# Performance work log

Hardware: AMD Instinct MI355X
Metric: run time of the kernel (lower is better)

The kernel has to match this reference:

```python
import jax, jax.numpy as jnp
import numpy as np

HIDDEN = 4544
NUM_HEADS = 71
HEAD_DIM = 64
ROPE_BASE = 10000.0


def _rope_cos_sin(seq_len, dim, dtype):
    inv_freq = 1.0 / (ROPE_BASE ** (jnp.arange(0, dim, 2, dtype=jnp.float32) / dim))
    t = jnp.arange(seq_len, dtype=jnp.float32)
    freqs = jnp.einsum('i,j->ij', t, inv_freq)            # [S, dim/2]
    emb = jnp.concatenate([freqs, freqs], axis=-1)        # [S, dim]
    return jnp.cos(emb).astype(dtype), jnp.sin(emb).astype(dtype)


def _rotate_half(x):
    half = x.shape[-1] // 2
    return jnp.concatenate([-x[..., half:], x[..., :half]], axis=-1)


def _apply_rope(x, cos, sin):
    # x: [..., S, hd]; cos/sin: [S, hd]
    return x * cos + _rotate_half(x) * sin


def setup_inputs() -> dict:
    key = jax.random.key(0)
    k1, k2, k3 = jax.random.split(key, 3)
    B, S = 1, 1024
    hidden_states = jax.random.normal(k1, (B, 1, S, HIDDEN), dtype=jnp.float32) * 0.02
    # additive causal mask (prefill)
    neg = jnp.triu(jnp.full((S, S), -1e9, dtype=jnp.float32), k=1)
    attention_mask = jnp.broadcast_to(neg[None, None], (B, 1, S, S))
    # fused QKV weight (already transposed for right-matmul): [H, (nh+2)*hd]
    qkv_w = jax.random.normal(k2, (HIDDEN, (NUM_HEADS + 2) * HEAD_DIM), dtype=jnp.float32) * 0.02
    dense_w = jax.random.normal(k3, (HIDDEN, HIDDEN), dtype=jnp.float32) * 0.02
    return {"hidden_states": hidden_states, "attention_mask": attention_mask,
            "qkv_w": qkv_w, "dense_w": dense_w}


def reference(hidden_states, attention_mask, qkv_w, dense_w):
    B, _, S, H = hidden_states.shape
    nh, hd = NUM_HEADS, HEAD_DIM
    x = hidden_states[:, 0]                               # [B, S, H]
    fused = jnp.einsum('bsh,hf->bsf', x, qkv_w)           # [B, S, (nh+2)*hd]
    fused = fused.reshape(B, S, nh + 2, hd)
    q = jnp.transpose(fused[:, :, :nh, :], (0, 2, 1, 3))  # [B, nh, S, hd]
    k = fused[:, :, nh, :]                                # [B, S, hd]  (single KV head, MQA)
    v = fused[:, :, nh + 1, :]                            # [B, S, hd]
    cos, sin = _rope_cos_sin(S, hd, q.dtype)
    q = _apply_rope(q, cos, sin)
    k = _apply_rope(k, cos, sin)
    scale = 1.0 / np.sqrt(hd).astype(np.float32)
    scores = jnp.einsum('bhsd,btd->bhst', q, k) * scale   # [B, nh, S, S]
    scores = scores + attention_mask                      # broadcast over heads
    probs = jax.nn.softmax(scores, axis=-1)
    ctx = jnp.einsum('bhst,btd->bhsd', probs, v)          # [B, nh, S, hd]
    ctx = jnp.transpose(ctx, (0, 2, 1, 3)).reshape(B, S, nh * hd)
    out = jnp.einsum('bsh,hg->bsg', ctx, dense_w)         # [B, S, H]
    return out[:, None]                                   # [B, 1, S, H]
```

## Files before the change

kernel.cpp:

```cpp
#include <hip/hip_runtime.h>

#define S_LEN 1024
#define HID   4544
#define NH    71
#define NQKV  4672

typedef __attribute__((ext_vector_type(4))) float f32x4;
typedef __attribute__((ext_vector_type(4))) unsigned short u16x4;
typedef __attribute__((ext_vector_type(8))) unsigned short u16x8;
typedef __attribute__((ext_vector_type(8))) __bf16 bf16x8;

__device__ __forceinline__ bf16x8 as_bf(u16x8 v) { return __builtin_bit_cast(bf16x8, v); }

__device__ __forceinline__ unsigned short f2bf(float f) {
    unsigned u = __builtin_bit_cast(unsigned, f);
    return (unsigned short)((u + 0x7FFFu + ((u >> 16) & 1u)) >> 16);
}
__device__ __forceinline__ float bf2f(unsigned short u) {
    return __builtin_bit_cast(float, (unsigned)u << 16);
}
__device__ __forceinline__ unsigned pk2(float a, float b) {
    return (unsigned)f2bf(a) | ((unsigned)f2bf(b) << 16);
}
__device__ __forceinline__ void gload16(const void* g, void* l) {
    __builtin_amdgcn_global_load_lds((const __attribute__((address_space(1))) unsigned int*)g,
                                     (__attribute__((address_space(3))) unsigned int*)l,
                                     16, 0, 0);
}

__global__ __launch_bounds__(256) void cvt_x_kernel(const float4* __restrict__ x,
                                                    ushort4* __restrict__ y) {
    int i = blockIdx.x * 256 + threadIdx.x;
    float4 v = x[i];
    ushort4 r;
    r.x = f2bf(v.x); r.y = f2bf(v.y); r.z = f2bf(v.z); r.w = f2bf(v.w);
    y[i] = r;
}

__global__ __launch_bounds__(256) void cvt_wT_kernel(const float* __restrict__ w,
                                                     unsigned short* __restrict__ wt,
                                                     int K, int N) {
    __shared__ float t[64][65];
    int n0 = blockIdx.x * 64, k0 = blockIdx.y * 64;
    int tx = threadIdx.x & 15, ty = threadIdx.x >> 4;
#pragma unroll
    for (int r = 0; r < 64; r += 16) {
        int k = k0 + ty + r;
        float4 v = *(const float4*)&w[(size_t)k * N + n0 + tx * 4];
        t[ty + r][tx * 4 + 0] = v.x;
        t[ty + r][tx * 4 + 1] = v.y;
        t[ty + r][tx * 4 + 2] = v.z;
        t[ty + r][tx * 4 + 3] = v.w;
    }
    __syncthreads();
    int nr = threadIdx.x >> 2;
    int kq = (threadIdx.x & 3) * 16;
    unsigned short tmp[16];
#pragma unroll
    for (int z = 0; z < 16; z++) tmp[z] = f2bf(t[kq + z][nr]);
    u16x8* dst = (u16x8*)&wt[(size_t)(n0 + nr) * K + k0 + kq];
    dst[0] = *(const u16x8*)&tmp[0];
    dst[1] = *(const u16x8*)&tmp[8];
}

__global__ void rope_table_kernel(float* __restrict__ cs, float* __restrict__ sn) {
    int s = blockIdx.x, i = threadIdx.x;
    float inv = powf(10000.0f, -(2.0f * (float)i) / 64.0f);
    float f = (float)s * inv;
    cs[s * 32 + i] = cosf(f);
    sn[s * 32 + i] = sinf(f);
}

template<int EPI>
__global__ __launch_bounds__(256, 3) void gemm_bt_kernel(
        const unsigned short* __restrict__ A, const unsigned short* __restrict__ BT,
        void* __restrict__ Cout, const float* __restrict__ cs_t,
        const float* __restrict__ sn_t, unsigned short* __restrict__ k_out,
        unsigned short* __restrict__ v_out, int K, int ldc) {
    __shared__ unsigned short As[2][128 * 64];
    __shared__ unsigned short Bs[2][64 * 64];
    int m0 = blockIdx.y * 128, n0 = blockIdx.x * 64;
    int t = threadIdx.x;
    int wv = t >> 6, lane = t & 63, lr = lane & 15, lg = lane >> 4;
    int mw = wv * 32;
    int sw = lr & 7;
    int srow = t >> 3, sc16 = t & 7;

    f32x4 acc[2][4];
#pragma unroll
    for (int mi = 0; mi < 2; mi++)
#pragma unroll
        for (int ni = 0; ni < 4; ni++) acc[mi][ni] = (f32x4)0.0f;

    const char* Ab = (const char*)A;
    const char* Bb = (const char*)BT;
    size_t rs = (size_t)K * 2;

    auto stage = [&](int step, int buf) {
        size_t kb = (size_t)step * 128;
#pragma unroll
        for (int i = 0; i < 4; i++) {
            int row = i * 32 + srow;
            int csrc = sc16 ^ (row & 7);
            gload16(Ab + (size_t)(m0 + row) * rs + kb + csrc * 16,
                    (char*)As[buf] + (i * 256 + t) * 16);
        }
#pragma unroll
        for (int i = 0; i < 2; i++) {
            int row = i * 32 + srow;
            int csrc = sc16 ^ (row & 7);
            gload16(Bb + (size_t)(n0 + row) * rs + kb + csrc * 16,
                    (char*)Bs[buf] + (i * 256 + t) * 16);
        }
    };

    stage(0, 0);
    __syncthreads();
    int nsteps = K >> 6;
    for (int s = 0; s < nsteps; ++s) {
        int cur = s & 1;
        if (s + 1 < nsteps) stage(s + 1, cur ^ 1);
        bf16x8 af[2][2], bfr[4][2];
#pragma unroll
        for (int mi = 0; mi < 2; mi++)
#pragma unroll
            for (int kk = 0; kk < 2; kk++) {
                int row = mw + mi * 16 + lr;
                af[mi][kk] = as_bf(*(const u16x8*)&As[cur][row * 64 + (((kk * 4 + lg) ^ sw) << 3)]);
            }
#pragma unroll
        for (int ni = 0; ni < 4; ni++)
#pragma unroll
            for (int kk = 0; kk < 2; kk++) {
                int row = ni * 16 + lr;
                bfr[ni][kk] = as_bf(*(const u16x8*)&Bs[cur][row * 64 + (((kk * 4 + lg) ^ sw) << 3)]);
            }
#pragma unroll
        for (int mi = 0; mi < 2; mi++)
#pragma unroll
            for (int ni = 0; ni < 4; ni++) {
                acc[mi][ni] = __builtin_amdgcn_mfma_f32_16x16x32_bf16(af[mi][0], bfr[ni][0], acc[mi][ni], 0, 0, 0);
                acc[mi][ni] = __builtin_amdgcn_mfma_f32_16x16x32_bf16(af[mi][1], bfr[ni][1], acc[mi][ni], 0, 0, 0);
            }
        __syncthreads();
    }

    if (EPI == 0) {
        float* C = (float*)Cout;
#pragma unroll
        for (int mi = 0; mi < 2; mi++)
#pragma unroll
            for (int ni = 0; ni < 4; ni++) {
                int col = n0 + ni * 16 + lr;
#pragma unroll
                for (int i = 0; i < 4; i++) {
                    int row = m0 + mw + mi * 16 + 4 * lg + i;
                    C[(size_t)row * ldc + col] = acc[mi][ni][i];
                }
            }
    } else {
        int hh = blockIdx.x;
        if (hh == 72) {
#pragma unroll
            for (int mi = 0; mi < 2; mi++)
#pragma unroll
                for (int ni = 0; ni < 4; ni++) {
                    int d = ni * 16 + lr;
                    int s0 = m0 + mw + mi * 16 + 4 * lg;
                    u16x4 pk;
#pragma unroll
                    for (int i = 0; i < 4; i++) pk[i] = f2bf(acc[mi][ni][i]);
                    *(u16x4*)&v_out[(size_t)d * S_LEN + s0] = pk;
                }
        } else {
            unsigned short* qb = (unsigned short*)Cout;
            float qscale = (hh < 71) ? 0.125f : 1.0f;
#pragma unroll
            for (int mi = 0; mi < 2; mi++)
#pragma unroll
                for (int i = 0; i < 4; i++) {
                    int s = m0 + mw + mi * 16 + 4 * lg + i;
                    float c0 = cs_t[s * 32 + lr],      g0 = sn_t[s * 32 + lr];
                    float c1 = cs_t[s * 32 + 16 + lr], g1 = sn_t[s * 32 + 16 + lr];
#pragma unroll
                    for (int ni = 0; ni < 4; ni++) {
                        float x  = acc[mi][ni][i];
                        float xp = acc[mi][ni ^ 2][i];
                        float c = (ni & 1) ? c1 : c0;
                        float g = (ni & 1) ? g1 : g0;
                        float r = (ni < 2) ? (x * c - xp * g) : (x * c + xp * g);
                        r *= qscale;
                        int d = ni * 16 + lr;
                        if (hh < 71) qb[(size_t)s * HID + hh * 64 + d] = f2bf(r);
                        else         k_out[(size_t)s * 64 + d] = f2bf(r);
                    }
                }
        }
    }
}

__global__ __launch_bounds__(256, 3) void attn_kernel(
        const unsigned short* __restrict__ qb, const unsigned short* __restrict__ kr,
        const unsigned short* __restrict__ vt, unsigned short* __restrict__ ctx,
        unsigned short* __restrict__ Opart, float2* __restrict__ MLpart) {
    __shared__ unsigned short Ks[2][64 * 64];
    __shared__ unsigned short Vs[2][64 * 64];
    __shared__ unsigned short Pl[4][16 * 72];
    int h = blockIdx.y;
    int u = blockIdx.x;
    int c, j0;
    if (u < 16)      { c = 0; j0 = u * 4; }
    else if (u < 28) { c = 1; j0 = 16 + (u - 16) * 4; }
    else if (u < 36) { c = 2; j0 = 32 + (u - 28) * 4; }
    else             { c = 3; j0 = 48 + (u - 36) * 4; }
    int t = threadIdx.x, wv = t >> 6, lane = t & 63, lr = lane & 15, lg = lane >> 4;
    int j = j0 + wv;
    int qs = j * 16 + lr;
    int k_lo = c * 256;
    int kend_w   = min((j + 1) * 16, k_lo + 256);
    int kend_max = min((j0 + 4) * 16, k_lo + 256);
    int nt = (kend_max - k_lo) >> 6;
    int nch = (j >> 4) + 1;
    int srow = t >> 3, sc16 = t & 7, sw = lr & 7;

    auto stage = [&](int ti, int buf) {
        size_t kbase = (size_t)(k_lo + ti * 64);
#pragma unroll
        for (int i = 0; i < 2; i++) {
            int row = i * 32 + srow;
            int csrc = sc16 ^ (row & 7);
            gload16((const char*)kr + (kbase + row) * 128 + csrc * 16,
                    (char*)Ks[buf] + (i * 256 + t) * 16);
        }
#pragma unroll
        for (int i = 0; i < 2; i++) {
            int row = i * 32 + srow;
            int csrc = sc16 ^ (row & 7);
            gload16((const char*)vt + (size_t)row * 2048 + kbase * 2 + csrc * 16,
                    (char*)Vs[buf] + (i * 256 + t) * 16);
        }
    };

    bf16x8 qf[2];
#pragma unroll
    for (int dc = 0; dc < 2; dc++)
        qf[dc] = as_bf(*(const u16x8*)&qb[(size_t)qs * HID + h * 64 + dc * 32 + 8 * lg]);

    float m_i = -1e30f, l_i = 0.0f;
    f32x4 o[4];
#pragma unroll
    for (int d4 = 0; d4 < 4; d4++) o[d4] = (f32x4)0.0f;

    stage(0, 0);
    __syncthreads();

    for (int ti = 0; ti < nt; ti++) {
        int cur = ti & 1;
        if (ti + 1 < nt) stage(ti + 1, cur ^ 1);
        int k0 = k_lo + ti * 64;
        if (k0 < kend_w) {
            f32x4 st[4];
#pragma unroll
            for (int nc = 0; nc < 4; nc++) st[nc] = (f32x4)0.0f;
#pragma unroll
            for (int nc = 0; nc < 4; nc++) {
                int krow = nc * 16 + lr;
#pragma unroll
                for (int dc = 0; dc < 2; dc++) {
                    bf16x8 kf = as_bf(*(const u16x8*)&Ks[cur][krow * 64 + (((dc * 4 + lg) ^ sw) << 3)]);
                    st[nc] = __builtin_amdgcn_mfma_f32_16x16x32_bf16(kf, qf[dc], st[nc], 0, 0, 0);
                }
            }
            bool needmask = (k0 + 64 > j * 16);
            float mx = -1e30f;
            if (needmask) {
#pragma unroll
                for (int nc = 0; nc < 4; nc++)
#pragma unroll
                    for (int i = 0; i < 4; i++) {
                        int ks = k0 + nc * 16 + 4 * lg + i;
                        float v = (ks <= qs) ? st[nc][i] : -1e30f;
                        st[nc][i] = v;
                        mx = fmaxf(mx, v);
                    }
            } else {
#pragma unroll
                for (int nc = 0; nc < 4; nc++)
#pragma unroll
                    for (int i = 0; i < 4; i++) mx = fmaxf(mx, st[nc][i]);
            }
            mx = fmaxf(mx, __shfl_xor(mx, 16));
            mx = fmaxf(mx, __shfl_xor(mx, 32));
            if (!__all(mx <= m_i + 8.0f)) {
                float mn = fmaxf(m_i, mx);
                float so = __expf(m_i - mn);
                l_i *= so;
#pragma unroll
                for (int d4 = 0; d4 < 4; d4++)
#pragma unroll
                    for (int i = 0; i < 4; i++) o[d4][i] *= so;
                m_i = mn;
            }
            float ps = 0.0f;
#pragma unroll
            for (int nc = 0; nc < 4; nc++)
#pragma unroll
                for (int i = 0; i < 4; i++) {
                    float v = st[nc][i];
                    float e = (!needmask || v > -1e29f) ? __expf(v - m_i) : 0.0f;
                    st[nc][i] = e;
                    ps += e;
                }
            ps += __shfl_xor(ps, 16);
            ps += __shfl_xor(ps, 32);
            l_i += ps;
#pragma unroll
            for (int nc = 0; nc < 4; nc++) {
                *(unsigned*)&Pl[wv][lr * 72 + nc * 16 + 4 * lg]     = pk2(st[nc][0], st[nc][1]);
                *(unsigned*)&Pl[wv][lr * 72 + nc * 16 + 4 * lg + 2] = pk2(st[nc][2], st[nc][3]);
            }
            bf16x8 pb[2];
#pragma unroll
            for (int kk = 0; kk < 2; kk++)
                pb[kk] = as_bf(*(const u16x8*)&Pl[wv][lr * 72 + kk * 32 + 8 * lg]);
#pragma unroll
            for (int d4 = 0; d4 < 4; d4++) {
                int vrow = d4 * 16 + lr;
#pragma unroll
                for (int kk = 0; kk < 2; kk++) {
                    bf16x8 vf = as_bf(*(const u16x8*)&Vs[cur][vrow * 64 + (((kk * 4 + lg) ^ sw) << 3)]);
                    o[d4] = __builtin_amdgcn_mfma_f32_16x16x32_bf16(vf, pb[kk], o[d4], 0, 0, 0);
                }
            }
        }
        __syncthreads();
    }

    if (nch == 1) {
        float linv = 1.0f / l_i;
#pragma unroll
        for (int d4 = 0; d4 < 4; d4++) {
            u16x4 pk;
#pragma unroll
            for (int i = 0; i < 4; i++) pk[i] = f2bf(o[d4][i] * linv);
            *(u16x4*)&ctx[(size_t)qs * HID + h * 64 + d4 * 16 + 4 * lg] = pk;
        }
    } else {
        int pi = (h * 48 + (j - 16)) * 4 + c;
#pragma unroll
        for (int d4 = 0; d4 < 4; d4++) {
            u16x4 pk;
#pragma unroll
            for (int i = 0; i < 4; i++) pk[i] = f2bf(o[d4][i]);
            *(u16x4*)&Opart[(size_t)pi * 1024 + lr * 64 + d4 * 16 + 4 * lg] = pk;
        }
        if (lg == 0) MLpart[pi * 16 + lr] = make_float2(m_i, l_i);
    }
}

__global__ __launch_bounds__(256) void merge_kernel(
        const unsigned short* __restrict__ Opart, const float2* __restrict__ MLpart,
        unsigned short* __restrict__ ctx) {
    int mu = blockIdx.x * 4 + (threadIdx.x >> 6);
    int lane = threadIdx.x & 63;
    int h = mu / 48, jj = mu % 48, j = 16 + jj;
    int nch = (j >> 4) + 1;
    int base = (h * 48 + jj) * 4;
    for (int q = 0; q < 16; q++) {
        float m[4], l[4], w[4];
        float M = -1e30f;
        for (int c = 0; c < nch; c++) {
            float2 ml = MLpart[(base + c) * 16 + q];
            m[c] = ml.x; l[c] = ml.y;
            M = fmaxf(M, m[c]);
        }
        float L = 0.0f;
        for (int c = 0; c < nch; c++) { w[c] = __expf(m[c] - M); L += l[c] * w[c]; }
        float acc = 0.0f;
        for (int c = 0; c < nch; c++)
            acc += w[c] * bf2f(Opart[(size_t)(base + c) * 1024 + q * 64 + lane]);
        ctx[(size_t)(j * 16 + q) * HID + h * 64 + lane] = f2bf(acc / L);
    }
}

extern "C" void kernel_launch(void* const* d_in, const int* in_sizes, int n_in,
                              void* d_out, int out_size, void* d_ws, size_t ws_size,
                              hipStream_t stream) {
    const float* hs      = (const float*)d_in[0];
    const float* qkv_w   = (const float*)d_in[2];
    const float* dense_w = (const float*)d_in[3];
    float* out = (float*)d_out;

    char* ws = (char*)d_ws;
    size_t off = 0;
    auto alloc = [&](size_t bytes) -> void* {
        void* p = ws + off;
        off += (bytes + 255) & ~(size_t)255;
        return p;
    };
    unsigned short* x_bf   = (unsigned short*)alloc((size_t)S_LEN * HID * 2);
    unsigned short* wqkvT  = (unsigned short*)alloc((size_t)NQKV * HID * 2);
    unsigned short* q_bf   = (unsigned short*)alloc((size_t)S_LEN * HID * 2);
    unsigned short* k_rope = (unsigned short*)alloc((size_t)S_LEN * 64 * 2);
    unsigned short* v_t    = (unsigned short*)alloc((size_t)64 * S_LEN * 2);
    unsigned short* ctx    = (unsigned short*)alloc((size_t)S_LEN * HID * 2);
    unsigned short* wdT    = (unsigned short*)alloc((size_t)HID * HID * 2);
    float*          cs_t   = (float*)alloc((size_t)S_LEN * 32 * 4);
    float*          sn_t   = (float*)alloc((size_t)S_LEN * 32 * 4);
    (void)ws_size;
    unsigned short* Opart  = wqkvT;
    float2*         MLpart = (float2*)((char*)wqkvT + (size_t)71 * 48 * 4 * 1024 * 2);

    cvt_x_kernel<<<dim3(S_LEN * HID / 1024), dim3(256), 0, stream>>>(
        (const float4*)hs, (ushort4*)x_bf);
    cvt_wT_kernel<<<dim3(NQKV / 64, HID / 64), dim3(256), 0, stream>>>(
        qkv_w, wqkvT, HID, NQKV);
    cvt_wT_kernel<<<dim3(HID / 64, HID / 64), dim3(256), 0, stream>>>(
        dense_w, wdT, HID, HID);
    rope_table_kernel<<<dim3(S_LEN), dim3(32), 0, stream>>>(cs_t, sn_t);

    gemm_bt_kernel<1><<<dim3(NQKV / 64, S_LEN / 128), dim3(256), 0, stream>>>(
        x_bf, wqkvT, q_bf, cs_t, sn_t, k_rope, v_t, HID, HID);

    attn_kernel<<<dim3(40, NH), dim3(256), 0, stream>>>(
        q_bf, k_rope, v_t, ctx, Opart, MLpart);

    merge_kernel<<<dim3(NH * 48 / 4), dim3(256), 0, stream>>>(Opart, MLpart, ctx);

    gemm_bt_kernel<0><<<dim3(HID / 64, S_LEN / 128), dim3(256), 0, stream>>>(
        ctx, wdT, out, nullptr, nullptr, nullptr, nullptr, HID, HID);
}
```

Measured before the change: 270.2 us.

## Split-K both GEMMs with XCD-aware block mapping and separate reduce kernels

Both GEMMs now split K into two halves and double the grid. Block indices are remapped so that the two K-halves and neighbouring M tiles land on chosen XCDs, which is meant to raise occupancy and improve L2 reuse. Partial fp32 results go to scratch buffers: the QKV partials into the dense-weight slot, with the dense weight transpose moved to run afterwards, and the dense partials into the QKV-weight slot. New reduce kernels then sum the halves, applying RoPE, scaling and the V transpose for QKV, or writing the output directly for the dense GEMM. The cost is extra fp32 traffic to write and reread the partials, plus two more kernel launches.

```diff
diff --git a/kernel.cpp b/kernel.cpp
--- a/kernel.cpp
+++ b/kernel.cpp
@@ -71,15 +71,18 @@
     sn[s * 32 + i] = sinf(f);
 }
 
-template<int EPI>
-__global__ __launch_bounds__(256, 3) void gemm_bt_kernel(
+__global__ __launch_bounds__(256, 3) void gemm_split_kernel(
         const unsigned short* __restrict__ A, const unsigned short* __restrict__ BT,
-        void* __restrict__ Cout, const float* __restrict__ cs_t,
-        const float* __restrict__ sn_t, unsigned short* __restrict__ k_out,
-        unsigned short* __restrict__ v_out, int K, int ldc) {
+        float* __restrict__ P, int N) {
     __shared__ unsigned short As[2][128 * 64];
     __shared__ unsigned short Bs[2][64 * 64];
-    int m0 = blockIdx.y * 128, n0 = blockIdx.x * 64;
+    int p = blockIdx.x;
+    int xcd = p & 7, idx = p >> 3;
+    int split = xcd & 1, mp = xcd >> 1;
+    int nbk = idx >> 1, m2 = idx & 1;
+    int m0 = (mp * 2 + m2) * 128, n0 = nbk * 64;
+    int s_begin = split ? 36 : 0;
+    int s_cnt   = split ? 35 : 36;
     int t = threadIdx.x;
     int wv = t >> 6, lane = t & 63, lr = lane & 15, lg = lane >> 4;
     int mw = wv * 32;
@@ -94,7 +97,7 @@
 
     const char* Ab = (const char*)A;
     const char* Bb = (const char*)BT;
-    size_t rs = (size_t)K * 2;
+    size_t rs = (size_t)HID * 2;
 
     auto stage = [&](int step, int buf) {
         size_t kb = (size_t)step * 128;
@@ -114,12 +117,11 @@
         }
     };
 
-    stage(0, 0);
+    stage(s_begin, 0);
     __syncthreads();
-    int nsteps = K >> 6;
-    for (int s = 0; s < nsteps; ++s) {
+    for (int s = 0; s < s_cnt; ++s) {
         int cur = s & 1;
-        if (s + 1 < nsteps) stage(s + 1, cur ^ 1);
+        if (s + 1 < s_cnt) stage(s_begin + s + 1, cur ^ 1);
         bf16x8 af[2][2], bfr[4][2];
 #pragma unroll
         for (int mi = 0; mi < 2; mi++)
@@ -145,58 +147,47 @@
         __syncthreads();
     }
 
-    if (EPI == 0) {
-        float* C = (float*)Cout;
-#pragma unroll
-        for (int mi = 0; mi < 2; mi++)
-#pragma unroll
-            for (int ni = 0; ni < 4; ni++) {
-                int col = n0 + ni * 16 + lr;
-#pragma unroll
-                for (int i = 0; i < 4; i++) {
-                    int row = m0 + mw + mi * 16 + 4 * lg + i;
-                    C[(size_t)row * ldc + col] = acc[mi][ni][i];
-                }
-            }
-    } else {
-        int hh = blockIdx.x;
-        if (hh == 72) {
-#pragma unroll
-            for (int mi = 0; mi < 2; mi++)
-#pragma unroll
-                for (int ni = 0; ni < 4; ni++) {
-                    int d = ni * 16 + lr;
-                    int s0 = m0 + mw + mi * 16 + 4 * lg;
-                    u16x4 pk;
-#pragma unroll
-                    for (int i = 0; i < 4; i++) pk[i] = f2bf(acc[mi][ni][i]);
-                    *(u16x4*)&v_out[(size_t)d * S_LEN + s0] = pk;
-                }
-        } else {
-            unsigned short* qb = (unsigned short*)Cout;
-            float qscale = (hh < 71) ? 0.125f : 1.0f;
-#pragma unroll
-            for (int mi = 0; mi < 2; mi++)
-#pragma unroll
-                for (int i = 0; i < 4; i++) {
-                    int s = m0 + mw + mi * 16 + 4 * lg + i;
-                    float c0 = cs_t[s * 32 + lr],      g0 = sn_t[s * 32 + lr];
-                    float c1 = cs_t[s * 32 + 16 + lr], g1 = sn_t[s * 32 + 16 + lr];
-#pragma unroll
-                    for (int ni = 0; ni < 4; ni++) {
-                        float x  = acc[mi][ni][i];
-                        float xp = acc[mi][ni ^ 2][i];
-                        float c = (ni & 1) ? c1 : c0;
-                        float g = (ni & 1) ? g1 : g0;
-                        float r = (ni < 2) ? (x * c - xp * g) : (x * c + xp * g);
-                        r *= qscale;
-                        int d = ni * 16 + lr;
-                        if (hh < 71) qb[(size_t)s * HID + hh * 64 + d] = f2bf(r);
-                        else         k_out[(size_t)s * 64 + d] = f2bf(r);
-                    }
-                }
-        }
-    }
+    float* C = P + (size_t)split * S_LEN * N;
+#pragma unroll
+    for (int mi = 0; mi < 2; mi++)
+#pragma unroll
+        for (int ni = 0; ni < 4; ni++) {
+            int col = n0 + ni * 16 + lr;
+#pragma unroll
+            for (int i = 0; i < 4; i++) {
+                int row = m0 + mw + mi * 16 + 4 * lg + i;
+                C[(size_t)row * N + col] = acc[mi][ni][i];
+            }
+        }
+}
+
+__global__ __launch_bounds__(256) void qkv_reduce_kernel(
+        const float* __restrict__ P1, const float* __restrict__ cs,
+        const float* __restrict__ sn, unsigned short* __restrict__ qb,
+        unsigned short* __restrict__ kr, unsigned short* __restrict__ vt) {
+    const size_t HALF = (size_t)S_LEN * NQKV;
+    int t = threadIdx.x;
+    int s = blockIdx.x * 4 + (t >> 6);
+    int hh = blockIdx.y, d = t & 63;
+    size_t base = (size_t)s * NQKV + hh * 64;
+    if (hh == 72) {
+        vt[(size_t)d * S_LEN + s] = f2bf(P1[base + d] + P1[HALF + base + d]);
+        return;
+    }
+    int i = d & 31;
+    float x  = P1[base + d]        + P1[HALF + base + d];
+    float xo = P1[base + (d ^ 32)] + P1[HALF + base + (d ^ 32)];
+    float c = cs[s * 32 + i], g = sn[s * 32 + i];
+    float r = x * c + ((d < 32) ? -xo : xo) * g;
+    if (hh == 71) kr[s * 64 + d] = f2bf(r);
+    else          qb[(size_t)s * HID + hh * 64 + d] = f2bf(r * 0.125f);
+}
+
+__global__ __launch_bounds__(256) void dense_reduce_kernel(
+        const f32x4* __restrict__ Pa, const f32x4* __restrict__ Pb,
+        f32x4* __restrict__ out) {
+    int i = blockIdx.x * 256 + threadIdx.x;
+    out[i] = Pa[i] + Pb[i];
 }
 
 __global__ __launch_bounds__(256, 3) void attn_kernel(
@@ -408,25 +399,31 @@
     float*          cs_t   = (float*)alloc((size_t)S_LEN * 32 * 4);
     float*          sn_t   = (float*)alloc((size_t)S_LEN * 32 * 4);
     (void)ws_size;
+    float*          P1     = (float*)wdT;
     unsigned short* Opart  = wqkvT;
     float2*         MLpart = (float2*)((char*)wqkvT + (size_t)71 * 48 * 4 * 1024 * 2);
+    float*          P2     = (float*)wqkvT;
 
     cvt_x_kernel<<<dim3(S_LEN * HID / 1024), dim3(256), 0, stream>>>(
         (const float4*)hs, (ushort4*)x_bf);
     cvt_wT_kernel<<<dim3(NQKV / 64, HID / 64), dim3(256), 0, stream>>>(
         qkv_w, wqkvT, HID, NQKV);
+    rope_table_kernel<<<dim3(S_LEN), dim3(32), 0, stream>>>(cs_t, sn_t);
+
+    gemm_split_kernel<<<dim3(16 * NQKV / 64), dim3(256), 0, stream>>>(
+        x_bf, wqkvT, P1, NQKV);
+    qkv_reduce_kernel<<<dim3(S_LEN / 4, NQKV / 64), dim3(256), 0, stream>>>(
+        P1, cs_t, sn_t, q_bf, k_rope, v_t);
+
     cvt_wT_kernel<<<dim3(HID / 64, HID / 64), dim3(256), 0, stream>>>(
         dense_w, wdT, HID, HID);
-    rope_table_kernel<<<dim3(S_LEN), dim3(32), 0, stream>>>(cs_t, sn_t);
-
-    gemm_bt_kernel<1><<<dim3(NQKV / 64, S_LEN / 128), dim3(256), 0, stream>>>(
-        x_bf, wqkvT, q_bf, cs_t, sn_t, k_rope, v_t, HID, HID);
 
     attn_kernel<<<dim3(40, NH), dim3(256), 0, stream>>>(
         q_bf, k_rope, v_t, ctx, Opart, MLpart);
-
     merge_kernel<<<dim3(NH * 48 / 4), dim3(256), 0, stream>>>(Opart, MLpart, ctx);
 
-    gemm_bt_kernel<0><<<dim3(HID / 64, S_LEN / 128), dim3(256), 0, stream>>>(
-        ctx, wdT, out, nullptr, nullptr, nullptr, nullptr, HID, HID);
-}
+    gemm_split_kernel<<<dim3(16 * HID / 64), dim3(256), 0, stream>>>(
+        ctx, wdT, P2, HID);
+    dense_reduce_kernel<<<dim3(S_LEN * HID / 1024), dim3(256), 0, stream>>>(
+        (const f32x4*)P2, (const f32x4*)(P2 + (size_t)S_LEN * HID), (f32x4*)out);
+}
```

Result: slower. 289.9 us (+7.3%).
